# Kernel tuning notes

Hardware: AMD Instinct MI355X
Metric: run time of the kernel (lower is better)

Reference implementation:

```python
import jax, jax.numpy as jnp
import numpy as np

NEG_INF = -1e9  # matches the torch module's masked_fill value of -1000000000.0


def setup_inputs() -> dict:
    key = jax.random.key(0)
    kq, kk, kv, km = jax.random.split(key, 4)
    b, h, L, d = 2, 16, 2048, 64
    q = jax.random.normal(kq, (b, h, L, d), dtype=jnp.float32)
    k = jax.random.normal(kk, (b, h, L, d), dtype=jnp.float32)
    v = jax.random.normal(kv, (b, h, L, d), dtype=jnp.float32)
    attn_mask = jax.random.randint(km, (b, 1, L, L), 0, 2, dtype=jnp.int32)
    return {"q": q, "k": k, "v": v, "attn_mask": attn_mask}


def reference(q, k, v, attn_mask):
    # att = q @ k^T / sqrt(d)   -> [b, h, Lq, Lk]
    scale = 1.0 / jnp.sqrt(jnp.asarray(q.shape[-1], q.dtype))
    att = jnp.einsum("bhqd,bhkd->bhqk", q, k) * scale
    # masked positions (mask == 0) filled with -1e9 before softmax
    att = jnp.where(attn_mask == 0, jnp.asarray(NEG_INF, att.dtype), att)
    att = jax.nn.softmax(att, axis=-1)
    # x = att @ v -> [b, h, Lq, d]
    return jnp.einsum("bhqk,bhkd->bhqd", att, v)
```

## Files before the change

### kernel.cpp

```cpp
#include <hip/hip_runtime.h>


typedef unsigned int u32;
typedef unsigned short u16;
typedef unsigned long long u64;

#define BH 32
#define Lseq 2048
#define Dh 64

#define KSCALE 0.125f
#define BIASF  -12.0f
#define NEGF   -1.0e9f

typedef __attribute__((ext_vector_type(8))) short frag_ab;
typedef __attribute__((ext_vector_type(16))) float f32x16;

__device__ __forceinline__ u16 f2bf(float f) {
    u32 u = __float_as_uint(f);
    u32 r = u + 0x7FFFu + ((u >> 16) & 1u);
    return (u16)(r >> 16);
}

__device__ __forceinline__ u32 cvtpk_bf16(float lo, float hi) {
    u32 r;
    asm("v_cvt_pk_bf16_f32 %0, %1, %2" : "=v"(r) : "v"(lo), "v"(hi));
    return r;
}

__device__ __forceinline__ void pl32swap(u32 &a, u32 &b) {
#if __has_builtin(__builtin_amdgcn_permlane32_swap)
    typedef __attribute__((ext_vector_type(2))) unsigned int uvec2;
    uvec2 r = __builtin_amdgcn_permlane32_swap(a, b, false, false);
    a = r[0]; b = r[1];
#else
    asm("v_permlane32_swap_b32 %0, %1" : "+v"(a), "+v"(b));
#endif
}

__device__ __forceinline__ void gl16(const void* g, void* l) {
    __builtin_amdgcn_global_load_lds(
        (const __attribute__((address_space(1))) u32*)g,
        (__attribute__((address_space(3))) u32*)l, 16, 0, 0);
}

__device__ __forceinline__ frag_ab mkfrag(u32 a, u32 b, u32 c, u32 d) {
    union { u32 w[4]; frag_ab f; } u;
    u.w[0] = a; u.w[1] = b; u.w[2] = c; u.w[3] = d;
    return u.f;
}

__global__ __launch_bounds__(256) void prep(
    const float* __restrict__ k, const float* __restrict__ v,
    const int* __restrict__ mask,
    u16* __restrict__ kb, u16* __restrict__ vtb, u64* __restrict__ bm)
{
    const int blk = blockIdx.x, tid = threadIdx.x;
    if (blk < 1024) {
        #pragma unroll
        for (int i = 0; i < 4; i++) {
            int u = blk * 1024 + i * 256 + tid;
            float4 f = ((const float4*)k)[u];
            ushort4 r;
            r.x = f2bf(f.x * KSCALE); r.y = f2bf(f.y * KSCALE);
            r.z = f2bf(f.z * KSCALE); r.w = f2bf(f.w * KSCALE);
            int dc  = (u >> 1) & 7;
            int key7 = (u >> 4) & 7;
            int u2 = (u & ~14) | (((dc ^ key7) & 7) << 1);
            ((ushort4*)kb)[u2] = r;
        }
    } else if (blk < 2048) {
        __shared__ u16 T[64 * 72];
        int job = blk - 1024;
        int bh = job >> 5, kt = job & 31;
        #pragma unroll
        for (int i = 0; i < 4; i++) {
            int idx = tid + 256 * i;
            int key = idx >> 4, ds = idx & 15;
            float4 f = *(const float4*)(v + ((size_t)(bh * Lseq + kt * 64 + key)) * Dh + ds * 4);
            int d0 = ds * 4;
            T[(d0 + 0) * 72 + key] = f2bf(f.x);
            T[(d0 + 1) * 72 + key] = f2bf(f.y);
            T[(d0 + 2) * 72 + key] = f2bf(f.z);
            T[(d0 + 3) * 72 + key] = f2bf(f.w);
        }
        __syncthreads();
        #pragma unroll
        for (int i = 0; i < 2; i++) {
            int cid = tid + 256 * i;
            int d = cid >> 3, kc = cid & 7;
            uint4 c = *(const uint4*)&T[d * 72 + kc * 8];
            *(uint4*)(vtb + ((size_t)(bh * Dh + d)) * Lseq + kt * 64 + ((kc ^ (d & 7)) * 8)) = c;
        }
    } else {
        int wv = (blk - 2048) * 4 + (tid >> 6);
        int lane = tid & 63;
        #pragma unroll
        for (int i = 0; i < 16; i++) {
            int widx = wv * 16 + i;
            int rowp = widx >> 5, kt = widx & 31;
            int val = mask[(size_t)rowp * Lseq + kt * 64 + lane];
            u64 bal = __ballot(val != 0);
            if (lane == 0) bm[(size_t)kt * 4096 + rowp] = bal;
        }
    }
}


#define STAGE(BUFOFS, KT) do {                                               \
    gl16(ktg0 + (size_t)(KT) * 4096,        smem_c + (BUFOFS) + tid * 16);   \
    gl16(ktg0 + (size_t)(KT) * 4096 + 2048, smem_c + (BUFOFS) + 4096 + tid * 16); \
    gl16(vtg0 + (KT) * 64,                  smem_c + (BUFOFS) + 8192 + tid * 16); \
    gl16(vtg0 + (KT) * 64 + 65536,          smem_c + (BUFOFS) + 12288 + tid * 16); \
} while (0)

#define KT_BODY(KT, CUR) {                                                   \
    u64 mw_nx = 0;                                                           \
    if ((KT) + 1 < 32) {                                                     \
        mw_nx = bm[(size_t)((KT) + 1) * 4096 + mrow];                        \
        STAGE((CUR) ^ 16384, (KT) + 1);                                      \
    }                                                                        \
    u64 sh = mw_cur >> sh4;                                                  \
    u32 w0 = (u32)sh, w1 = (u32)(sh >> 32);                                  \
    frag_ab kf0[4], kf1[4];                                                  \
    _Pragma("unroll")                                                        \
    for (int ko = 0; ko < 4; ko++) {                                         \
        kf0[ko] = *(const frag_ab*)(smem_c + (CUR) + kaddr[ko]);             \
        kf1[ko] = *(const frag_ab*)(smem_c + (CUR) + 4096 + kaddr[ko]);      \
    }                                                                        \
    f32x16 s0, s1;                                                           \
    _Pragma("unroll")                                                        \
    for (int r = 0; r < 16; r++) {                                           \
        const int bit = (r & 3) + 8 * (r >> 2);                              \
        s0[r] = (w0 & (1u << bit)) ? BIASF : NEGF;                           \
        s1[r] = (w1 & (1u << bit)) ? BIASF : NEGF;                           \
    }                                                                        \
    __builtin_amdgcn_s_setprio(1);                                           \
    _Pragma("unroll")                                                        \
    for (int ko = 0; ko < 4; ko++) {                                         \
        s0 = __builtin_amdgcn_mfma_f32_32x32x16_bf16(kf0[ko], qf[ko], s0, 0, 0, 0); \
        s1 = __builtin_amdgcn_mfma_f32_32x32x16_bf16(kf1[ko], qf[ko], s1, 0, 0, 0); \
    }                                                                        \
    __builtin_amdgcn_s_setprio(0);                                           \
    u32 y0[8], y1[8];                                                        \
    _Pragma("unroll")                                                        \
    for (int j = 0; j < 8; j++) {                                            \
        float pa = __expf(s0[2 * j]);                                        \
        float pb = __expf(s0[2 * j + 1]);                                    \
        float pc = __expf(s1[2 * j]);                                        \
        float pd = __expf(s1[2 * j + 1]);                                    \
        l_run += (pa + pb) + (pc + pd);                                      \
        y0[j] = cvtpk_bf16(pa, pb);                                          \
        y1[j] = cvtpk_bf16(pc, pd);                                          \
    }                                                                        \
    pl32swap(y0[0], y0[2]); pl32swap(y0[1], y0[3]);                          \
    pl32swap(y0[4], y0[6]); pl32swap(y0[5], y0[7]);                          \
    pl32swap(y1[0], y1[2]); pl32swap(y1[1], y1[3]);                          \
    pl32swap(y1[4], y1[6]); pl32swap(y1[5], y1[7]);                          \
    frag_ab pf[4];                                                           \
    pf[0] = mkfrag(y0[0], y0[1], y0[2], y0[3]);                              \
    pf[1] = mkfrag(y0[4], y0[5], y0[6], y0[7]);                              \
    pf[2] = mkfrag(y1[0], y1[1], y1[2], y1[3]);                              \
    pf[3] = mkfrag(y1[4], y1[5], y1[6], y1[7]);                              \
    __builtin_amdgcn_s_setprio(1);                                           \
    _Pragma("unroll")                                                        \
    for (int ks = 0; ks < 4; ks++) {                                         \
        frag_ab va = *(const frag_ab*)(smem_c + (CUR) + vaddr[ks]);          \
        frag_ab vb = *(const frag_ab*)(smem_c + (CUR) + 4096 + vaddr[ks]);   \
        o0 = __builtin_amdgcn_mfma_f32_32x32x16_bf16(va, pf[ks], o0, 0, 0, 0); \
        o1 = __builtin_amdgcn_mfma_f32_32x32x16_bf16(vb, pf[ks], o1, 0, 0, 0); \
    }                                                                        \
    __builtin_amdgcn_s_setprio(0);                                           \
    __syncthreads();                                                         \
    mw_cur = mw_nx;                                                          \
}

__global__ __launch_bounds__(256, 2)
void attn_mfma(const float* __restrict__ qg, const u16* __restrict__ kb,
               const u16* __restrict__ vtb, const u64* __restrict__ bm,
               float* __restrict__ outg)
{
    const int bid = blockIdx.x;
    const int swz = (bid & 7) * 64 + (bid >> 3);
    const int bh = swz >> 4, b = bh >> 4;
    const int q0 = (swz & 15) * 128;
    const int tid = threadIdx.x;
    const int wave = tid >> 6, lane = tid & 63;
    const int ql = lane & 31, hi = lane >> 5;
    const int sh4 = hi * 4;

    __shared__ u16 smem[16384];
    char* smem_c = (char*)smem;

    const u16* ktg0 = kb + ((size_t)bh << 17) + tid * 8;
    const u16* vtg0 = vtb + ((size_t)bh << 17) + ((tid >> 3) << 11) + (tid & 7) * 8;

    STAGE(0, 0);

    frag_ab qf[4];
    #pragma unroll
    for (int ko = 0; ko < 4; ko++) {
        const float* p = qg + ((size_t)bh * Lseq + q0 + 32 * wave + ql) * Dh + ko * 16 + 8 * hi;
        float4 f0 = *(const float4*)p;
        float4 f1 = *(const float4*)(p + 4);
        union { u32 w[4]; frag_ab f; } uq;
        uq.w[0] = (u32)f2bf(f0.x) | ((u32)f2bf(f0.y) << 16);
        uq.w[1] = (u32)f2bf(f0.z) | ((u32)f2bf(f0.w) << 16);
        uq.w[2] = (u32)f2bf(f1.x) | ((u32)f2bf(f1.y) << 16);
        uq.w[3] = (u32)f2bf(f1.z) | ((u32)f2bf(f1.w) << 16);
        qf[ko] = uq.f;
    }

    int kaddr[4], vaddr[4];
    #pragma unroll
    for (int j = 0; j < 4; j++) {
        int chunk = ((j << 1) | hi) ^ (ql & 7);
        kaddr[j] = ql * 128 + chunk * 16;
        vaddr[j] = 8192 + ql * 128 + chunk * 16;
    }

    const int mrow = b * 2048 + q0 + 32 * wave + ql;
    u64 mw_cur = bm[mrow];

    f32x16 o0, o1;
    #pragma unroll
    for (int i = 0; i < 16; i++) { o0[i] = 0.f; o1[i] = 0.f; }
    float l_run = 0.f;

    __syncthreads();

    #pragma unroll 1
    for (int kt0 = 0; kt0 < 32; kt0 += 2) {
        KT_BODY(kt0, 0)
        KT_BODY(kt0 + 1, 16384)
    }

    float l = l_run;
    l += __shfl_xor(l, 32);
    const float inv = 1.0f / l;
    float* orow = outg + ((size_t)bh * Lseq + q0 + 32 * wave + ql) * Dh;
    #pragma unroll
    for (int q4 = 0; q4 < 4; q4++) {
        *(float4*)(orow + 8 * q4 + 4 * hi) =
            make_float4(o0[4 * q4 + 0] * inv, o0[4 * q4 + 1] * inv,
                        o0[4 * q4 + 2] * inv, o0[4 * q4 + 3] * inv);
        *(float4*)(orow + 32 + 8 * q4 + 4 * hi) =
            make_float4(o1[4 * q4 + 0] * inv, o1[4 * q4 + 1] * inv,
                        o1[4 * q4 + 2] * inv, o1[4 * q4 + 3] * inv);
    }
}

extern "C" void kernel_launch(void* const* d_in, const int* in_sizes, int n_in,
                              void* d_out, int out_size, void* d_ws, size_t ws_size,
                              hipStream_t stream) {
    const float* q    = (const float*)d_in[0];
    const float* k    = (const float*)d_in[1];
    const float* v    = (const float*)d_in[2];
    const int*   mask = (const int*)d_in[3];
    float* out = (float*)d_out;

    char* ws = (char*)d_ws;
    u16* kb  = (u16*)(ws);
    u16* vtb = (u16*)(ws + 8388608);
    u64* bmp = (u64*)(ws + 16777216);

    hipLaunchKernelGGL(prep, dim3(4096), dim3(256), 0, stream, k, v, mask, kb, vtb, bmp);
    hipLaunchKernelGGL(attn_mfma, dim3(512), dim3(256), 0, stream,
                       q, kb, vtb, bmp, out);
}
```

Baseline: 174.8 us.

## Software-pipeline QK and PV across tiles with 4-stage LDS ring buffer

New measurement: 170.6 us. 1.02x faster.

```diff
diff --git a/kernel.cpp b/kernel.cpp
--- a/kernel.cpp
+++ b/kernel.cpp
@@ -107,27 +107,28 @@
 }
 
 
-#define STAGE(BUFOFS, KT) do {                                               \
-    gl16(ktg0 + (size_t)(KT) * 4096,        smem_c + (BUFOFS) + tid * 16);   \
-    gl16(ktg0 + (size_t)(KT) * 4096 + 2048, smem_c + (BUFOFS) + 4096 + tid * 16); \
-    gl16(vtg0 + (KT) * 64,                  smem_c + (BUFOFS) + 8192 + tid * 16); \
-    gl16(vtg0 + (KT) * 64 + 65536,          smem_c + (BUFOFS) + 12288 + tid * 16); \
+#define STAGE(BUF, KT) do {                                                  \
+    gl16(ktg0 + (size_t)(KT) * 4096,        smem_c + ((BUF) << 14) + tid * 16);        \
+    gl16(ktg0 + (size_t)(KT) * 4096 + 2048, smem_c + ((BUF) << 14) + 4096 + tid * 16); \
+    gl16(vtg0 + (KT) * 64,                  smem_c + ((BUF) << 14) + 8192 + tid * 16); \
+    gl16(vtg0 + (KT) * 64 + 65536,          smem_c + ((BUF) << 14) + 12288 + tid * 16);\
 } while (0)
 
-#define KT_BODY(KT, CUR) {                                                   \
-    u64 mw_nx = 0;                                                           \
-    if ((KT) + 1 < 32) {                                                     \
-        mw_nx = bm[(size_t)((KT) + 1) * 4096 + mrow];                        \
-        STAGE((CUR) ^ 16384, (KT) + 1);                                      \
-    }                                                                        \
-    u64 sh = mw_cur >> sh4;                                                  \
+#define PV_CLUSTER(BV, PF) {                                                 \
+    __builtin_amdgcn_s_setprio(1);                                           \
+    _Pragma("unroll")                                                        \
+    for (int ks = 0; ks < 4; ks++) {                                         \
+        frag_ab va = *(const frag_ab*)(smem_c + ((BV) << 14) + vaddr[ks]);   \
+        frag_ab vb = *(const frag_ab*)(smem_c + ((BV) << 14) + 4096 + vaddr[ks]); \
+        o0 = __builtin_amdgcn_mfma_f32_32x32x16_bf16(va, PF[ks], o0, 0, 0, 0); \
+        o1 = __builtin_amdgcn_mfma_f32_32x32x16_bf16(vb, PF[ks], o1, 0, 0, 0); \
+    }                                                                        \
+    __builtin_amdgcn_s_setprio(0);                                           \
+}
+
+#define QK_EXP(BKX, MW, PF_EX) {                                             \
+    u64 sh = (MW) >> sh4;                                                    \
     u32 w0 = (u32)sh, w1 = (u32)(sh >> 32);                                  \
-    frag_ab kf0[4], kf1[4];                                                  \
-    _Pragma("unroll")                                                        \
-    for (int ko = 0; ko < 4; ko++) {                                         \
-        kf0[ko] = *(const frag_ab*)(smem_c + (CUR) + kaddr[ko]);             \
-        kf1[ko] = *(const frag_ab*)(smem_c + (CUR) + 4096 + kaddr[ko]);      \
-    }                                                                        \
     f32x16 s0, s1;                                                           \
     _Pragma("unroll")                                                        \
     for (int r = 0; r < 16; r++) {                                           \
@@ -138,8 +139,10 @@
     __builtin_amdgcn_s_setprio(1);                                           \
     _Pragma("unroll")                                                        \
     for (int ko = 0; ko < 4; ko++) {                                         \
-        s0 = __builtin_amdgcn_mfma_f32_32x32x16_bf16(kf0[ko], qf[ko], s0, 0, 0, 0); \
-        s1 = __builtin_amdgcn_mfma_f32_32x32x16_bf16(kf1[ko], qf[ko], s1, 0, 0, 0); \
+        frag_ab kf0 = *(const frag_ab*)(smem_c + ((BKX) << 14) + kaddr[ko]); \
+        frag_ab kf1 = *(const frag_ab*)(smem_c + ((BKX) << 14) + 4096 + kaddr[ko]); \
+        s0 = __builtin_amdgcn_mfma_f32_32x32x16_bf16(kf0, qf[ko], s0, 0, 0, 0); \
+        s1 = __builtin_amdgcn_mfma_f32_32x32x16_bf16(kf1, qf[ko], s1, 0, 0, 0); \
     }                                                                        \
     __builtin_amdgcn_s_setprio(0);                                           \
     u32 y0[8], y1[8];                                                        \
@@ -157,22 +160,20 @@
     pl32swap(y0[4], y0[6]); pl32swap(y0[5], y0[7]);                          \
     pl32swap(y1[0], y1[2]); pl32swap(y1[1], y1[3]);                          \
     pl32swap(y1[4], y1[6]); pl32swap(y1[5], y1[7]);                          \
-    frag_ab pf[4];                                                           \
-    pf[0] = mkfrag(y0[0], y0[1], y0[2], y0[3]);                              \
-    pf[1] = mkfrag(y0[4], y0[5], y0[6], y0[7]);                              \
-    pf[2] = mkfrag(y1[0], y1[1], y1[2], y1[3]);                              \
-    pf[3] = mkfrag(y1[4], y1[5], y1[6], y1[7]);                              \
-    __builtin_amdgcn_s_setprio(1);                                           \
-    _Pragma("unroll")                                                        \
-    for (int ks = 0; ks < 4; ks++) {                                         \
-        frag_ab va = *(const frag_ab*)(smem_c + (CUR) + vaddr[ks]);          \
-        frag_ab vb = *(const frag_ab*)(smem_c + (CUR) + 4096 + vaddr[ks]);   \
-        o0 = __builtin_amdgcn_mfma_f32_32x32x16_bf16(va, pf[ks], o0, 0, 0, 0); \
-        o1 = __builtin_amdgcn_mfma_f32_32x32x16_bf16(vb, pf[ks], o1, 0, 0, 0); \
-    }                                                                        \
-    __builtin_amdgcn_s_setprio(0);                                           \
+    PF_EX[0] = mkfrag(y0[0], y0[1], y0[2], y0[3]);                           \
+    PF_EX[1] = mkfrag(y0[4], y0[5], y0[6], y0[7]);                           \
+    PF_EX[2] = mkfrag(y1[0], y1[1], y1[2], y1[3]);                           \
+    PF_EX[3] = mkfrag(y1[4], y1[5], y1[6], y1[7]);                           \
+}
+
+#define KT_BODY(KT, BK1, BV, BS, PF_PV, PF_EX, MW_USE, MW_LD, HASN2) {       \
+    if (HASN2) {                                                             \
+        MW_LD = bm[(size_t)((KT) + 2) * 4096 + mrow];                        \
+        STAGE(BS, (KT) + 2);                                                 \
+    }                                                                        \
+    PV_CLUSTER(BV, PF_PV)                                                    \
+    QK_EXP(BK1, MW_USE, PF_EX)                                               \
     __syncthreads();                                                         \
-    mw_cur = mw_nx;                                                          \
 }
 
 __global__ __launch_bounds__(256, 2)
@@ -189,13 +190,19 @@
     const int ql = lane & 31, hi = lane >> 5;
     const int sh4 = hi * 4;
 
-    __shared__ u16 smem[16384];
+    __shared__ u16 smem[32768];
     char* smem_c = (char*)smem;
 
     const u16* ktg0 = kb + ((size_t)bh << 17) + tid * 8;
     const u16* vtg0 = vtb + ((size_t)bh << 17) + ((tid >> 3) << 11) + (tid & 7) * 8;
 
     STAGE(0, 0);
+    STAGE(1, 1);
+
+    const int mrow = b * 2048 + q0 + 32 * wave + ql;
+    u64 mwp = bm[mrow];
+    u64 mwB = bm[(size_t)4096 + mrow];
+    u64 mwA = 0;
 
     frag_ab qf[4];
     #pragma unroll
@@ -219,21 +226,29 @@
         vaddr[j] = 8192 + ql * 128 + chunk * 16;
     }
 
-    const int mrow = b * 2048 + q0 + 32 * wave + ql;
-    u64 mw_cur = bm[mrow];
-
     f32x16 o0, o1;
     #pragma unroll
     for (int i = 0; i < 16; i++) { o0[i] = 0.f; o1[i] = 0.f; }
     float l_run = 0.f;
 
+    frag_ab pfA[4], pfB[4];
+
     __syncthreads();
 
+    { QK_EXP(0, mwp, pfA) }
+
     #pragma unroll 1
-    for (int kt0 = 0; kt0 < 32; kt0 += 2) {
-        KT_BODY(kt0, 0)
-        KT_BODY(kt0 + 1, 16384)
-    }
+    for (int kt = 0; kt < 28; kt += 4) {
+        KT_BODY(kt + 0, 1, 0, 2, pfA, pfB, mwB, mwA, 1)
+        KT_BODY(kt + 1, 2, 1, 3, pfB, pfA, mwA, mwB, 1)
+        KT_BODY(kt + 2, 3, 2, 0, pfA, pfB, mwB, mwA, 1)
+        KT_BODY(kt + 3, 0, 3, 1, pfB, pfA, mwA, mwB, 1)
+    }
+    KT_BODY(28, 1, 0, 2, pfA, pfB, mwB, mwA, 1)
+    KT_BODY(29, 2, 1, 3, pfB, pfA, mwA, mwB, 1)
+    KT_BODY(30, 3, 2, 0, pfA, pfB, mwB, mwA, 0)
+
+    PV_CLUSTER(3, pfB)
 
     float l = l_run;
     l += __shfl_xor(l, 32);
```

## Prelayout K/V in MFMA fragment order and load directly to registers, dropping LDS

Applied to the files above, without the earlier changes.

Result: no change. 174.3 us (-0.3%).

```diff
diff --git a/kernel.cpp b/kernel.cpp
--- a/kernel.cpp
+++ b/kernel.cpp
@@ -20,6 +20,10 @@
     u32 u = __float_as_uint(f);
     u32 r = u + 0x7FFFu + ((u >> 16) & 1u);
     return (u16)(r >> 16);
+}
+
+__device__ __forceinline__ u32 pk2bf(float a, float b) {
+    return (u32)f2bf(a) | ((u32)f2bf(b) << 16);
 }
 
 __device__ __forceinline__ u32 cvtpk_bf16(float lo, float hi) {
@@ -38,12 +42,6 @@
 #endif
 }
 
-__device__ __forceinline__ void gl16(const void* g, void* l) {
-    __builtin_amdgcn_global_load_lds(
-        (const __attribute__((address_space(1))) u32*)g,
-        (__attribute__((address_space(3))) u32*)l, 16, 0, 0);
-}
-
 __device__ __forceinline__ frag_ab mkfrag(u32 a, u32 b, u32 c, u32 d) {
     union { u32 w[4]; frag_ab f; } u;
     u.w[0] = a; u.w[1] = b; u.w[2] = c; u.w[3] = d;
@@ -53,21 +51,26 @@
 __global__ __launch_bounds__(256) void prep(
     const float* __restrict__ k, const float* __restrict__ v,
     const int* __restrict__ mask,
-    u16* __restrict__ kb, u16* __restrict__ vtb, u64* __restrict__ bm)
+    u16* __restrict__ kfm, u16* __restrict__ vfm, u64* __restrict__ bm)
 {
     const int blk = blockIdx.x, tid = threadIdx.x;
     if (blk < 1024) {
-        #pragma unroll
-        for (int i = 0; i < 4; i++) {
-            int u = blk * 1024 + i * 256 + tid;
-            float4 f = ((const float4*)k)[u];
-            ushort4 r;
-            r.x = f2bf(f.x * KSCALE); r.y = f2bf(f.y * KSCALE);
-            r.z = f2bf(f.z * KSCALE); r.w = f2bf(f.w * KSCALE);
-            int dc  = (u >> 1) & 7;
-            int key7 = (u >> 4) & 7;
-            int u2 = (u & ~14) | (((dc ^ key7) & 7) << 1);
-            ((ushort4*)kb)[u2] = r;
+        const int bh = blk >> 5, kt = blk & 31;
+        #pragma unroll
+        for (int i = 0; i < 2; i++) {
+            int cid = tid + 256 * i;
+            int half = cid >> 8, ko = (cid >> 6) & 3, lane = cid & 63;
+            int key = kt * 64 + half * 32 + (lane & 31);
+            int d0 = ko * 16 + 8 * (lane >> 5);
+            const float* src = k + ((size_t)(bh * Lseq + key)) * Dh + d0;
+            float4 f0 = *(const float4*)src;
+            float4 f1 = *(const float4*)(src + 4);
+            uint4 o;
+            o.x = pk2bf(f0.x * KSCALE, f0.y * KSCALE);
+            o.y = pk2bf(f0.z * KSCALE, f0.w * KSCALE);
+            o.z = pk2bf(f1.x * KSCALE, f1.y * KSCALE);
+            o.w = pk2bf(f1.z * KSCALE, f1.w * KSCALE);
+            *(uint4*)(kfm + ((size_t)(blk * 8 + half * 4 + ko) * 64 + lane) * 8) = o;
         }
     } else if (blk < 2048) {
         __shared__ u16 T[64 * 72];
@@ -88,9 +91,11 @@
         #pragma unroll
         for (int i = 0; i < 2; i++) {
             int cid = tid + 256 * i;
-            int d = cid >> 3, kc = cid & 7;
-            uint4 c = *(const uint4*)&T[d * 72 + kc * 8];
-            *(uint4*)(vtb + ((size_t)(bh * Dh + d)) * Lseq + kt * 64 + ((kc ^ (d & 7)) * 8)) = c;
+            int dhalf = cid >> 8, ks = (cid >> 6) & 3, lane = cid & 63;
+            int d = dhalf * 32 + (lane & 31);
+            int koff = ks * 16 + 8 * (lane >> 5);
+            uint4 c = *(const uint4*)&T[d * 72 + koff];
+            *(uint4*)(vfm + ((size_t)(job * 8 + dhalf * 4 + ks) * 64 + lane) * 8) = c;
         }
     } else {
         int wv = (blk - 2048) * 4 + (tid >> 6);
@@ -107,27 +112,21 @@
 }
 
 
-#define STAGE(BUFOFS, KT) do {                                               \
-    gl16(ktg0 + (size_t)(KT) * 4096,        smem_c + (BUFOFS) + tid * 16);   \
-    gl16(ktg0 + (size_t)(KT) * 4096 + 2048, smem_c + (BUFOFS) + 4096 + tid * 16); \
-    gl16(vtg0 + (KT) * 64,                  smem_c + (BUFOFS) + 8192 + tid * 16); \
-    gl16(vtg0 + (KT) * 64 + 65536,          smem_c + (BUFOFS) + 12288 + tid * 16); \
-} while (0)
-
-#define KT_BODY(KT, CUR) {                                                   \
-    u64 mw_nx = 0;                                                           \
-    if ((KT) + 1 < 32) {                                                     \
-        mw_nx = bm[(size_t)((KT) + 1) * 4096 + mrow];                        \
-        STAGE((CUR) ^ 16384, (KT) + 1);                                      \
-    }                                                                        \
-    u64 sh = mw_cur >> sh4;                                                  \
+#define LDK(DST, KT) {                                                       \
+    _Pragma("unroll")                                                        \
+    for (int j = 0; j < 8; j++)                                              \
+        DST[j] = *(const frag_ab*)(kbase + ((KT) * 8 + j) * 512);            \
+}
+
+#define BODY(KT, KC, KN, MW, HASK, HASM) {                                   \
+    frag_ab vf[8];                                                           \
+    _Pragma("unroll")                                                        \
+    for (int j = 0; j < 8; j++)                                              \
+        vf[j] = *(const frag_ab*)(vbase + ((KT) * 8 + j) * 512);             \
+    if (HASK) LDK(KN, (KT) + 1)                                              \
+    u64 sh = (MW) >> sh4;                                                    \
     u32 w0 = (u32)sh, w1 = (u32)(sh >> 32);                                  \
-    frag_ab kf0[4], kf1[4];                                                  \
-    _Pragma("unroll")                                                        \
-    for (int ko = 0; ko < 4; ko++) {                                         \
-        kf0[ko] = *(const frag_ab*)(smem_c + (CUR) + kaddr[ko]);             \
-        kf1[ko] = *(const frag_ab*)(smem_c + (CUR) + 4096 + kaddr[ko]);      \
-    }                                                                        \
+    if (HASM) MW = bm[(size_t)((KT) + 2) * 4096 + mrow];                     \
     f32x16 s0, s1;                                                           \
     _Pragma("unroll")                                                        \
     for (int r = 0; r < 16; r++) {                                           \
@@ -138,8 +137,8 @@
     __builtin_amdgcn_s_setprio(1);                                           \
     _Pragma("unroll")                                                        \
     for (int ko = 0; ko < 4; ko++) {                                         \
-        s0 = __builtin_amdgcn_mfma_f32_32x32x16_bf16(kf0[ko], qf[ko], s0, 0, 0, 0); \
-        s1 = __builtin_amdgcn_mfma_f32_32x32x16_bf16(kf1[ko], qf[ko], s1, 0, 0, 0); \
+        s0 = __builtin_amdgcn_mfma_f32_32x32x16_bf16(KC[ko],     qf[ko], s0, 0, 0, 0); \
+        s1 = __builtin_amdgcn_mfma_f32_32x32x16_bf16(KC[4 + ko], qf[ko], s1, 0, 0, 0); \
     }                                                                        \
     __builtin_amdgcn_s_setprio(0);                                           \
     u32 y0[8], y1[8];                                                        \
@@ -165,19 +164,15 @@
     __builtin_amdgcn_s_setprio(1);                                           \
     _Pragma("unroll")                                                        \
     for (int ks = 0; ks < 4; ks++) {                                         \
-        frag_ab va = *(const frag_ab*)(smem_c + (CUR) + vaddr[ks]);          \
-        frag_ab vb = *(const frag_ab*)(smem_c + (CUR) + 4096 + vaddr[ks]);   \
-        o0 = __builtin_amdgcn_mfma_f32_32x32x16_bf16(va, pf[ks], o0, 0, 0, 0); \
-        o1 = __builtin_amdgcn_mfma_f32_32x32x16_bf16(vb, pf[ks], o1, 0, 0, 0); \
+        o0 = __builtin_amdgcn_mfma_f32_32x32x16_bf16(vf[ks],     pf[ks], o0, 0, 0, 0); \
+        o1 = __builtin_amdgcn_mfma_f32_32x32x16_bf16(vf[4 + ks], pf[ks], o1, 0, 0, 0); \
     }                                                                        \
     __builtin_amdgcn_s_setprio(0);                                           \
-    __syncthreads();                                                         \
-    mw_cur = mw_nx;                                                          \
 }
 
 __global__ __launch_bounds__(256, 2)
-void attn_mfma(const float* __restrict__ qg, const u16* __restrict__ kb,
-               const u16* __restrict__ vtb, const u64* __restrict__ bm,
+void attn_mfma(const float* __restrict__ qg, const u16* __restrict__ kfm,
+               const u16* __restrict__ vfm, const u64* __restrict__ bm,
                float* __restrict__ outg)
 {
     const int bid = blockIdx.x;
@@ -189,13 +184,15 @@
     const int ql = lane & 31, hi = lane >> 5;
     const int sh4 = hi * 4;
 
-    __shared__ u16 smem[16384];
-    char* smem_c = (char*)smem;
-
-    const u16* ktg0 = kb + ((size_t)bh << 17) + tid * 8;
-    const u16* vtg0 = vtb + ((size_t)bh << 17) + ((tid >> 3) << 11) + (tid & 7) * 8;
-
-    STAGE(0, 0);
+    const u16* kbase = kfm + ((size_t)bh << 17) + lane * 8;
+    const u16* vbase = vfm + ((size_t)bh << 17) + lane * 8;
+
+    const int mrow = b * 2048 + q0 + 32 * wave + ql;
+
+    frag_ab kA[8], kB[8];
+    LDK(kA, 0)
+    u64 mwE = bm[mrow];
+    u64 mwO = bm[(size_t)4096 + mrow];
 
     frag_ab qf[4];
     #pragma unroll
@@ -204,36 +201,25 @@
         float4 f0 = *(const float4*)p;
         float4 f1 = *(const float4*)(p + 4);
         union { u32 w[4]; frag_ab f; } uq;
-        uq.w[0] = (u32)f2bf(f0.x) | ((u32)f2bf(f0.y) << 16);
-        uq.w[1] = (u32)f2bf(f0.z) | ((u32)f2bf(f0.w) << 16);
-        uq.w[2] = (u32)f2bf(f1.x) | ((u32)f2bf(f1.y) << 16);
-        uq.w[3] = (u32)f2bf(f1.z) | ((u32)f2bf(f1.w) << 16);
+        uq.w[0] = pk2bf(f0.x, f0.y);
+        uq.w[1] = pk2bf(f0.z, f0.w);
+        uq.w[2] = pk2bf(f1.x, f1.y);
+        uq.w[3] = pk2bf(f1.z, f1.w);
         qf[ko] = uq.f;
     }
-
-    int kaddr[4], vaddr[4];
-    #pragma unroll
-    for (int j = 0; j < 4; j++) {
-        int chunk = ((j << 1) | hi) ^ (ql & 7);
-        kaddr[j] = ql * 128 + chunk * 16;
-        vaddr[j] = 8192 + ql * 128 + chunk * 16;
-    }
-
-    const int mrow = b * 2048 + q0 + 32 * wave + ql;
-    u64 mw_cur = bm[mrow];
 
     f32x16 o0, o1;
     #pragma unroll
     for (int i = 0; i < 16; i++) { o0[i] = 0.f; o1[i] = 0.f; }
     float l_run = 0.f;
 
-    __syncthreads();
-
     #pragma unroll 1
-    for (int kt0 = 0; kt0 < 32; kt0 += 2) {
-        KT_BODY(kt0, 0)
-        KT_BODY(kt0 + 1, 16384)
-    }
+    for (int kt = 0; kt < 30; kt += 2) {
+        BODY(kt,     kA, kB, mwE, 1, 1)
+        BODY(kt + 1, kB, kA, mwO, 1, 1)
+    }
+    BODY(30, kA, kB, mwE, 1, 0)
+    BODY(31, kB, kA, mwO, 0, 0)
 
     float l = l_run;
     l += __shfl_xor(l, 32);
@@ -260,11 +246,11 @@
     float* out = (float*)d_out;
 
     char* ws = (char*)d_ws;
-    u16* kb  = (u16*)(ws);
-    u16* vtb = (u16*)(ws + 8388608);
+    u16* kfm = (u16*)(ws);
+    u16* vfm = (u16*)(ws + 8388608);
     u64* bmp = (u64*)(ws + 16777216);
 
-    hipLaunchKernelGGL(prep, dim3(4096), dim3(256), 0, stream, k, v, mask, kb, vtb, bmp);
+    hipLaunchKernelGGL(prep, dim3(4096), dim3(256), 0, stream, k, v, mask, kfm, vfm, bmp);
     hipLaunchKernelGGL(attn_mfma, dim3(512), dim3(256), 0, stream,
-                       q, kb, vtb, bmp, out);
-}
+                       q, kfm, vfm, bmp, out);
+}
```
